# Optimization experiments

Hardware: AMD Instinct MI355X
Metric: run time of the kernel (lower is better)

Reference implementation:

```python
import jax, jax.numpy as jnp
import numpy as np

B_, L, D = 4, 2048, 1024          # batch, seq_len, d_model
E = 2 * D                         # d_inner (expand=2)
N = 8                             # d_state
K = 4                             # d_conv
R = D // 16                       # dt_rank = 64
EPS = 1e-5


def silu(x):
    return x * jax.nn.sigmoid(x)


def setup_inputs() -> dict:
    key = jax.random.key(0)
    ks = jax.random.split(key, 8)
    s = 0.02
    inp = jax.random.normal(ks[0], (B_, L, D), jnp.float32)
    in_proj_w = jax.random.normal(ks[1], (2 * E, D), jnp.float32) * s
    conv_w = jax.random.normal(ks[2], (E, 1, K), jnp.float32) * s  # depthwise, OIW
    conv_b = jnp.zeros((E,), jnp.float32)
    x_proj_w = jax.random.normal(ks[3], (R + 2 * N, E), jnp.float32) * s
    dt_proj_w = jax.random.normal(ks[4], (E, R), jnp.float32) * s
    # bias so softplus(dt) gives realistic small timesteps
    dt_proj_b = jax.random.uniform(ks[5], (E,), jnp.float32, minval=-4.0, maxval=-2.0)
    # S4D-real init: A = -[1..N] per channel
    A_log = jnp.log(jnp.broadcast_to(jnp.arange(1, N + 1, dtype=jnp.float32), (E, N)))
    D_param = jnp.ones((E,), jnp.float32)
    out_proj_w = jax.random.normal(ks[6], (D, E), jnp.float32) * s
    rms_w = jnp.ones((D,), jnp.float32)
    return dict(inp=inp, in_proj_w=in_proj_w, conv_w=conv_w, conv_b=conv_b,
                x_proj_w=x_proj_w, dt_proj_w=dt_proj_w, dt_proj_b=dt_proj_b,
                A_log=A_log, D_param=D_param, out_proj_w=out_proj_w, rms_w=rms_w)


def reference(inp, in_proj_w, conv_w, conv_b, x_proj_w, dt_proj_w, dt_proj_b,
              A_log, D_param, out_proj_w, rms_w):
    b, l, d = inp.shape
    # input projection -> x (ssm branch) and z (gate branch), each (b, l, E)
    xz = inp @ in_proj_w.T
    x, z = jnp.split(xz, 2, axis=-1)
    # depthwise causal conv1d along time
    xt = x.transpose(0, 2, 1)                                   # (b, E, l)
    xc = jax.lax.conv_general_dilated(xt, conv_w, (1,), [(K - 1, 0)],
                                      feature_group_count=E)
    x = silu((xc + conv_b[None, :, None]).transpose(0, 2, 1))   # (b, l, E)
    # data-dependent SSM params
    dbc = x @ x_proj_w.T                                        # (b, l, R+2N)
    dt, Bm, Cm = jnp.split(dbc, [R, R + N], axis=-1)
    delta = jax.nn.softplus(dt @ dt_proj_w.T + dt_proj_b)       # (b, l, E)
    A = -jnp.exp(A_log)                                         # (E, N)

    def step(h, t):
        d_t, B_t, C_t, u_t = t                                  # (b,E),(b,N),(b,N),(b,E)
        dA = jnp.exp(d_t[..., None] * A)                        # (b, E, N)
        h = h * dA + (d_t * u_t)[..., None] * B_t[:, None, :]
        y = jnp.einsum('ben,bn->be', h, C_t)
        return h, y

    xs = (delta.transpose(1, 0, 2), Bm.transpose(1, 0, 2),
          Cm.transpose(1, 0, 2), x.transpose(1, 0, 2))
    h0 = jnp.zeros((b, E, N), inp.dtype)
    _, ys = jax.lax.scan(step, h0, xs)                          # ys: (l, b, E)
    y = ys.transpose(1, 0, 2) + x * D_param                     # skip term u*D
    y = y * silu(z)                                             # gating
    out = y @ out_proj_w.T                                      # (b, l, D)
    # RMSNorm
    out = out * jax.lax.rsqrt(jnp.mean(out * out, axis=-1, keepdims=True) + EPS) * rms_w
    # dropout p=0 -> identity
    return out
```

## Files before the change

### kernel.cpp

```cpp
#include <hip/hip_runtime.h>

#define LL 2048
#define EE 2048
#define DD 1024
#define NC 32
#define CH 64

typedef short bf16x8 __attribute__((ext_vector_type(8)));
typedef float f32x4 __attribute__((ext_vector_type(4)));

__device__ inline float bf2f(unsigned short u) {
    union { unsigned u; float f; } v; v.u = ((unsigned)u) << 16; return v.f;
}
__device__ inline unsigned short f2bf(float f) {
    union { float f; unsigned u; } v; v.f = f;
    unsigned r = v.u + 0x7fff + ((v.u >> 16) & 1);
    return (unsigned short)(r >> 16);
}

__device__ inline void gload_lds16(const void* g, void* lds) {
    __builtin_amdgcn_global_load_lds(
        (const __attribute__((address_space(1))) unsigned int*)g,
        (__attribute__((address_space(3))) unsigned int*)lds, 16, 0, 0);
}

template<int MODE, int BN>
__global__ __launch_bounds__(512, 2)
void gemm8p(const unsigned short* __restrict__ A,
            const unsigned short* __restrict__ Bw,
            void* __restrict__ Cout,
            const float* __restrict__ bias,
            int M, int N, int K)
{
    constexpr int NREP = BN / 64;
    constexpr int RB   = BN / 128;
    constexpr int LH   = 2 + RB;
    constexpr int NSTRIP = BN / 4;

    extern __shared__ short lds[];
    short* Asm = lds;
    short* Bsm = lds + 2 * 2 * 256 * 32;

    const int tid = threadIdx.x;
    const int w = tid >> 6, lane = tid & 63;
    const int wm = w >> 2, wn = w & 3;

    const int gx = N / BN;
    const int nwg = gx * (M / 256);
    int lin = blockIdx.y * gx + blockIdx.x;
    int swz = ((nwg & 7) == 0) ? ((lin & 7) * (nwg >> 3) + (lin >> 3)) : lin;
    const long m0 = (long)(swz / gx) * 256;
    const long n0 = (long)(swz % gx) * BN;

    const int g = (tid & 3) ^ ((tid >> 3) & 3);
    const int arow = tid >> 2;
    const unsigned short* Ag = A + (m0 + arow) * (long)K + g * 8;
    const unsigned short* Bg = Bw + (n0 + arow) * (long)K + g * 8;
    const int ldsrow = w * 16;

    auto stageA = [&](int buf, int kh, int j, int kt) {
        gload_lds16(Ag + (long)j * 128 * K + kt * 64 + kh * 32,
                    Asm + ((buf * 2 + kh) * 256 + j * 128 + ldsrow) * 32);
    };
    auto stageB = [&](int buf, int kh, int j, int kt) {
        gload_lds16(Bg + (long)j * 128 * K + kt * 64 + kh * 32,
                    Bsm + ((buf * 2 + kh) * BN + j * 128 + ldsrow) * 32);
    };

    f32x4 acc[8][NREP] = {};

    stageA(0, 0, 0, 0); stageA(0, 0, 1, 0);
#pragma unroll
    for (int j = 0; j < RB; ++j) stageB(0, 0, j, 0);
    stageA(0, 1, 0, 0); stageA(0, 1, 1, 0);
#pragma unroll
    for (int j = 0; j < RB; ++j) stageB(0, 1, j, 0);

    const int NT = K / 64;
    const int rr = lane & 15;
    const int sl = ((lane >> 4) ^ ((rr >> 1) & 3)) * 8;

    for (int t = 0; t < NT; ++t) {
        const int cur = t & 1, nxt = cur ^ 1;
        const bool more = (t + 1 < NT);

        asm volatile("s_waitcnt vmcnt(%0)" :: "i"(LH) : "memory");
        __builtin_amdgcn_s_barrier();

        const short* Ac0 = Asm + (cur * 2 + 0) * 256 * 32;
        const short* Bc0 = Bsm + (cur * 2 + 0) * BN * 32;
        if (more) { stageA(nxt, 0, 0, t + 1); stageA(nxt, 0, 1, t + 1); }
        bf16x8 a[4], b[NREP];
#pragma unroll
        for (int m = 0; m < 4; ++m)
            a[m] = *(const bf16x8*)&Ac0[(wm * 128 + m * 16 + rr) * 32 + sl];
#pragma unroll
        for (int n = 0; n < NREP; ++n)
            b[n] = *(const bf16x8*)&Bc0[(wn * NSTRIP + n * 16 + rr) * 32 + sl];
        __builtin_amdgcn_s_setprio(1);
#pragma unroll
        for (int m = 0; m < 4; ++m)
#pragma unroll
            for (int n = 0; n < NREP; ++n)
                acc[m][n] = __builtin_amdgcn_mfma_f32_16x16x32_bf16(a[m], b[n], acc[m][n], 0, 0, 0);
        __builtin_amdgcn_s_setprio(0);
        if (more) {
#pragma unroll
            for (int j = 0; j < RB; ++j) stageB(nxt, 0, j, t + 1);
        }
#pragma unroll
        for (int m = 0; m < 4; ++m)
            a[m] = *(const bf16x8*)&Ac0[(wm * 128 + 64 + m * 16 + rr) * 32 + sl];
        __builtin_amdgcn_s_setprio(1);
#pragma unroll
        for (int m = 0; m < 4; ++m)
#pragma unroll
            for (int n = 0; n < NREP; ++n)
                acc[4 + m][n] = __builtin_amdgcn_mfma_f32_16x16x32_bf16(a[m], b[n], acc[4 + m][n], 0, 0, 0);
        __builtin_amdgcn_s_setprio(0);

        if (more) { asm volatile("s_waitcnt vmcnt(%0)" :: "i"(LH) : "memory"); }
        else      { asm volatile("s_waitcnt vmcnt(0)" ::: "memory"); }
        __builtin_amdgcn_s_barrier();

        const short* Ac1 = Asm + (cur * 2 + 1) * 256 * 32;
        const short* Bc1 = Bsm + (cur * 2 + 1) * BN * 32;
        if (more) { stageA(nxt, 1, 0, t + 1); stageA(nxt, 1, 1, t + 1); }
#pragma unroll
        for (int m = 0; m < 4; ++m)
            a[m] = *(const bf16x8*)&Ac1[(wm * 128 + m * 16 + rr) * 32 + sl];
#pragma unroll
        for (int n = 0; n < NREP; ++n)
            b[n] = *(const bf16x8*)&Bc1[(wn * NSTRIP + n * 16 + rr) * 32 + sl];
        __builtin_amdgcn_s_setprio(1);
#pragma unroll
        for (int m = 0; m < 4; ++m)
#pragma unroll
            for (int n = 0; n < NREP; ++n)
                acc[m][n] = __builtin_amdgcn_mfma_f32_16x16x32_bf16(a[m], b[n], acc[m][n], 0, 0, 0);
        __builtin_amdgcn_s_setprio(0);
        if (more) {
#pragma unroll
            for (int j = 0; j < RB; ++j) stageB(nxt, 1, j, t + 1);
        }
#pragma unroll
        for (int m = 0; m < 4; ++m)
            a[m] = *(const bf16x8*)&Ac1[(wm * 128 + 64 + m * 16 + rr) * 32 + sl];
        __builtin_amdgcn_s_setprio(1);
#pragma unroll
        for (int m = 0; m < 4; ++m)
#pragma unroll
            for (int n = 0; n < NREP; ++n)
                acc[4 + m][n] = __builtin_amdgcn_mfma_f32_16x16x32_bf16(a[m], b[n], acc[4 + m][n], 0, 0, 0);
        __builtin_amdgcn_s_setprio(0);
    }

#pragma unroll
    for (int m = 0; m < 8; ++m) {
#pragma unroll
        for (int n = 0; n < NREP; ++n) {
#pragma unroll
            for (int r = 0; r < 4; ++r) {
                long row = m0 + wm * 128 + m * 16 + (lane >> 4) * 4 + r;
                long col = n0 + wn * NSTRIP + n * 16 + (lane & 15);
                float v = acc[m][n][r];
                if (MODE == 0) {
                    ((float*)Cout)[row * N + col] = v;
                } else if (MODE == 1) {
                    ((unsigned short*)Cout)[row * N + col] = f2bf(v);
                } else {
                    v += bias[col];
                    float sp = (v > 20.f) ? v : log1pf(__expf(v));
                    ((unsigned short*)Cout)[row * N + col] = f2bf(sp);
                }
            }
        }
    }
}

template<int MODE>
__global__ __launch_bounds__(256)
void gemm_bt(const unsigned short* __restrict__ A,
             const unsigned short* __restrict__ Bw,
             void* __restrict__ Cout,
             unsigned short* __restrict__ dt_out,
             int M, int N, int K)
{
    __shared__ short As[128 * 32];
    __shared__ short Bs[128 * 32];
    const int tid = threadIdx.x;
    const int wave = tid >> 6, lane = tid & 63;
    const int wm = wave >> 1, wn = wave & 1;
    const long m0 = (long)blockIdx.y * 128;
    const long n0 = (long)blockIdx.x * 128;

    f32x4 acc[4][4] = {};

    const int srow = lane >> 2;
    const int skoff = (lane & 3) * 8;
    const int c0 = wave, c1 = wave + 4;

    for (int k0 = 0; k0 < K; k0 += 32) {
        gload_lds16(A + (m0 + c0 * 16 + srow) * (long)K + k0 + skoff, &As[c0 * 16 * 32]);
        gload_lds16(A + (m0 + c1 * 16 + srow) * (long)K + k0 + skoff, &As[c1 * 16 * 32]);
        gload_lds16(Bw + (n0 + c0 * 16 + srow) * (long)K + k0 + skoff, &Bs[c0 * 16 * 32]);
        gload_lds16(Bw + (n0 + c1 * 16 + srow) * (long)K + k0 + skoff, &Bs[c1 * 16 * 32]);
        __syncthreads();

        bf16x8 af[4], bfr[4];
#pragma unroll
        for (int m = 0; m < 4; ++m)
            af[m] = *(const bf16x8*)&As[(wm * 64 + m * 16 + (lane & 15)) * 32 + (lane >> 4) * 8];
#pragma unroll
        for (int n = 0; n < 4; ++n)
            bfr[n] = *(const bf16x8*)&Bs[(wn * 64 + n * 16 + (lane & 15)) * 32 + (lane >> 4) * 8];
#pragma unroll
        for (int m = 0; m < 4; ++m)
#pragma unroll
            for (int n = 0; n < 4; ++n)
                acc[m][n] = __builtin_amdgcn_mfma_f32_16x16x32_bf16(af[m], bfr[n], acc[m][n], 0, 0, 0);
        __syncthreads();
    }

#pragma unroll
    for (int m = 0; m < 4; ++m) {
#pragma unroll
        for (int n = 0; n < 4; ++n) {
#pragma unroll
            for (int r = 0; r < 4; ++r) {
                long row = m0 + wm * 64 + m * 16 + (lane >> 4) * 4 + r;
                long col = n0 + wn * 64 + n * 16 + (lane & 15);
                float v = acc[m][n][r];
                ((float*)Cout)[row * N + col] = v;
                if (MODE == 3) {
                    if (col < 64) dt_out[row * 64 + col] = f2bf(v);
                }
            }
        }
    }
}

__global__ void cvt_f32_bf16(const float* __restrict__ in, unsigned short* __restrict__ out, long n) {
    long i = ((long)blockIdx.x * blockDim.x + threadIdx.x) * 4;
    long stride = (long)gridDim.x * blockDim.x * 4;
    for (; i < n; i += stride) {
        float4 v = *(const float4*)(in + i);
        out[i + 0] = f2bf(v.x); out[i + 1] = f2bf(v.y);
        out[i + 2] = f2bf(v.z); out[i + 3] = f2bf(v.w);
    }
}

__global__ void cvt_pad_xproj(const float* __restrict__ in, unsigned short* __restrict__ out) {
    int i = blockIdx.x * 256 + threadIdx.x;
    int r = i >> 11, c = i & 2047;
    out[i] = (r < 80) ? f2bf(in[r * 2048 + c]) : (unsigned short)0;
}

__global__ void conv_silu_k(const unsigned short* __restrict__ xz,
                            const float* __restrict__ cw,
                            const float* __restrict__ cb,
                            unsigned short* __restrict__ xc)
{
    const int e = blockIdx.y * 256 + threadIdx.x;
    const int b = blockIdx.z;
    const int l0 = blockIdx.x * 128;
    const float w0 = cw[e * 4 + 0], w1 = cw[e * 4 + 1], w2 = cw[e * 4 + 2], w3 = cw[e * 4 + 3];
    const float bias = cb[e];
    const unsigned short* xrow = xz + (long)b * LL * 4096 + e;
    unsigned short* orow = xc + (long)b * LL * 2048 + e;
    float xm3 = (l0 >= 3) ? bf2f(xrow[(long)(l0 - 3) * 4096]) : 0.f;
    float xm2 = (l0 >= 2) ? bf2f(xrow[(long)(l0 - 2) * 4096]) : 0.f;
    float xm1 = (l0 >= 1) ? bf2f(xrow[(long)(l0 - 1) * 4096]) : 0.f;
    for (int l = l0; l < l0 + 128; ++l) {
        float x0 = bf2f(xrow[(long)l * 4096]);
        float v = bias + w0 * xm3 + w1 * xm2 + w2 * xm1 + w3 * x0;
        float s = v / (1.f + __expf(-v));
        orow[(long)l * 2048] = f2bf(s);
        xm3 = xm2; xm2 = xm1; xm1 = x0;
    }
}

__global__ __launch_bounds__(256)
void scan_local(const unsigned short* __restrict__ delta,
                const unsigned short* __restrict__ xconv,
                const float* __restrict__ dbc,
                const float* __restrict__ A_log,
                float* __restrict__ hend, float* __restrict__ Ssum)
{
    const int e = blockIdx.x * 256 + threadIdx.x;
    const int c = blockIdx.y, b = blockIdx.z;
    const int l0 = c * CH;
    float An[8];
#pragma unroll
    for (int n = 0; n < 8; ++n) An[n] = -__expf(A_log[e * 8 + n]);
    float h[8] = {};
    float S = 0.f;
    const unsigned short* drow = delta + ((long)b * LL + l0) * EE + e;
    const unsigned short* urow = xconv + ((long)b * LL + l0) * EE + e;
    const float* bc = dbc + ((long)b * LL + l0) * 128;
    for (int l = 0; l < CH; ++l) {
        float d = bf2f(drow[(long)l * EE]);
        float u = bf2f(urow[(long)l * EE]);
        float du = d * u;
        S += d;
#pragma unroll
        for (int n = 0; n < 8; ++n)
            h[n] = h[n] * __expf(d * An[n]) + du * bc[l * 128 + 64 + n];
    }
    const long o = ((long)b * NC + c) * EE + e;
#pragma unroll
    for (int n = 0; n < 8; ++n) hend[o * 8 + n] = h[n];
    Ssum[o] = S;
}

__global__ __launch_bounds__(256)
void scan_combine(const float* __restrict__ hend, const float* __restrict__ Ssum,
                  const float* __restrict__ A_log, float* __restrict__ hin)
{
    const int t = blockIdx.x * 256 + threadIdx.x;
    const int b = t >> 11, e = t & 2047;
    float An[8];
#pragma unroll
    for (int n = 0; n < 8; ++n) An[n] = -__expf(A_log[e * 8 + n]);
    float h[8] = {};
    for (int c = 0; c < NC; ++c) {
        const long o = ((long)b * NC + c) * EE + e;
#pragma unroll
        for (int n = 0; n < 8; ++n) hin[o * 8 + n] = h[n];
        float S = Ssum[o];
#pragma unroll
        for (int n = 0; n < 8; ++n)
            h[n] = h[n] * __expf(An[n] * S) + hend[o * 8 + n];
    }
}

__global__ __launch_bounds__(256)
void scan_final(const unsigned short* __restrict__ delta,
                const unsigned short* __restrict__ xconv,
                const float* __restrict__ dbc,
                const unsigned short* __restrict__ xz,
                const float* __restrict__ A_log,
                const float* __restrict__ Dparam,
                const float* __restrict__ hin,
                unsigned short* __restrict__ yg)
{
    const int e = blockIdx.x * 256 + threadIdx.x;
    const int c = blockIdx.y, b = blockIdx.z;
    const int l0 = c * CH;
    float An[8];
#pragma unroll
    for (int n = 0; n < 8; ++n) An[n] = -__expf(A_log[e * 8 + n]);
    const float Dp = Dparam[e];
    float h[8];
    const long o = ((long)b * NC + c) * EE + e;
#pragma unroll
    for (int n = 0; n < 8; ++n) h[n] = hin[o * 8 + n];
    const unsigned short* drow = delta + ((long)b * LL + l0) * EE + e;
    const unsigned short* urow = xconv + ((long)b * LL + l0) * EE + e;
    const unsigned short* zrow = xz + ((long)b * LL + l0) * 4096 + 2048 + e;
    const float* bc = dbc + ((long)b * LL + l0) * 128;
    unsigned short* yrow = yg + ((long)b * LL + l0) * EE + e;
    for (int l = 0; l < CH; ++l) {
        float d = bf2f(drow[(long)l * EE]);
        float u = bf2f(urow[(long)l * EE]);
        float du = d * u;
        float y = 0.f;
#pragma unroll
        for (int n = 0; n < 8; ++n) {
            h[n] = h[n] * __expf(d * An[n]) + du * bc[l * 128 + 64 + n];
            y += h[n] * bc[l * 128 + 72 + n];
        }
        y += u * Dp;
        float z = bf2f(zrow[(long)l * 4096]);
        float g = z / (1.f + __expf(-z));
        yrow[(long)l * EE] = f2bf(y * g);
    }
}

__global__ __launch_bounds__(256)
void rmsnorm_k(const float* __restrict__ in, const float* __restrict__ w, float* __restrict__ out) {
    const int row = blockIdx.x;
    const float4* r4 = (const float4*)(in + (long)row * 1024);
    float4 v = r4[threadIdx.x];
    float ss = v.x * v.x + v.y * v.y + v.z * v.z + v.w * v.w;
#pragma unroll
    for (int m = 32; m >= 1; m >>= 1) ss += __shfl_xor(ss, m, 64);
    __shared__ float wsum[4];
    const int wave = threadIdx.x >> 6;
    if ((threadIdx.x & 63) == 0) wsum[wave] = ss;
    __syncthreads();
    float tot = wsum[0] + wsum[1] + wsum[2] + wsum[3];
    float sc = rsqrtf(tot * (1.f / 1024.f) + 1e-5f);
    float4 wv = ((const float4*)w)[threadIdx.x];
    float4 o;
    o.x = v.x * sc * wv.x; o.y = v.y * sc * wv.y;
    o.z = v.z * sc * wv.z; o.w = v.w * sc * wv.w;
    ((float4*)(out + (long)row * 1024))[threadIdx.x] = o;
}

extern "C" void kernel_launch(void* const* d_in, const int* in_sizes, int n_in,
                              void* d_out, int out_size, void* d_ws, size_t ws_size,
                              hipStream_t stream)
{
    const float* inp   = (const float*)d_in[0];
    const float* w_in  = (const float*)d_in[1];
    const float* convw = (const float*)d_in[2];
    const float* convb = (const float*)d_in[3];
    const float* w_xp  = (const float*)d_in[4];
    const float* w_dt  = (const float*)d_in[5];
    const float* b_dt  = (const float*)d_in[6];
    const float* A_log = (const float*)d_in[7];
    const float* Dp    = (const float*)d_in[8];
    const float* w_out = (const float*)d_in[9];
    const float* rmsw  = (const float*)d_in[10];

    char* ws = (char*)d_ws;
    const size_t MB = 1024 * 1024;
    unsigned short* inp_bf   = (unsigned short*)(ws + 0);
    unsigned short* win_bf   = (unsigned short*)(ws + 16 * MB);
    unsigned short* xz_bf    = (unsigned short*)(ws + 24 * MB);
    unsigned short* xconv_bf = (unsigned short*)(ws + 88 * MB);
    unsigned short* wxp_bf   = (unsigned short*)(ws + 120 * MB);
    float*          dbc      = (float*)(ws + 121 * MB);
    unsigned short* dt_bf    = (unsigned short*)(ws + 125 * MB);
    unsigned short* wdt_bf   = (unsigned short*)(ws + 126 * MB);
    unsigned short* delta_bf = (unsigned short*)(ws + 127 * MB);
    unsigned short* yg_bf    = (unsigned short*)(ws + 191 * MB);
    unsigned short* wout_bf  = (unsigned short*)(ws + 223 * MB);
    float*          hend     = (float*)(ws + 0);
    float*          hin      = (float*)(ws + 8 * MB);
    float*          Ssum     = (float*)(ws + 16 * MB);
    float*          out_pre  = (float*)(ws + 0);

    hipFuncSetAttribute((const void*)gemm8p<1, 256>, hipFuncAttributeMaxDynamicSharedMemorySize, 131072);
    hipFuncSetAttribute((const void*)gemm8p<2, 128>, hipFuncAttributeMaxDynamicSharedMemorySize, 98304);
    hipFuncSetAttribute((const void*)gemm8p<0, 128>, hipFuncAttributeMaxDynamicSharedMemorySize, 98304);

    cvt_f32_bf16<<<2048, 256, 0, stream>>>(inp, inp_bf, (long)8192 * 1024);
    cvt_f32_bf16<<<2048, 256, 0, stream>>>(w_in, win_bf, (long)4096 * 1024);
    cvt_pad_xproj<<<1024, 256, 0, stream>>>(w_xp, wxp_bf);
    cvt_f32_bf16<<<512, 256, 0, stream>>>(w_dt, wdt_bf, (long)2048 * 64);
    cvt_f32_bf16<<<2048, 256, 0, stream>>>(w_out, wout_bf, (long)1024 * 2048);

    gemm8p<1, 256><<<dim3(16, 32), 512, 131072, stream>>>(inp_bf, win_bf, xz_bf, nullptr, 8192, 4096, 1024);
    conv_silu_k<<<dim3(16, 8, 4), 256, 0, stream>>>(xz_bf, convw, convb, xconv_bf);
    gemm_bt<3><<<dim3(1, 64), 256, 0, stream>>>(xconv_bf, wxp_bf, dbc, dt_bf, 8192, 128, 2048);
    gemm8p<2, 128><<<dim3(16, 32), 512, 98304, stream>>>(dt_bf, wdt_bf, delta_bf, b_dt, 8192, 2048, 64);
    scan_local<<<dim3(8, NC, 4), 256, 0, stream>>>(delta_bf, xconv_bf, dbc, A_log, hend, Ssum);
    scan_combine<<<32, 256, 0, stream>>>(hend, Ssum, A_log, hin);
    scan_final<<<dim3(8, NC, 4), 256, 0, stream>>>(delta_bf, xconv_bf, dbc, xz_bf, A_log, Dp, hin, yg_bf);
    gemm8p<0, 128><<<dim3(8, 32), 512, 98304, stream>>>(yg_bf, wout_bf, out_pre, nullptr, 8192, 1024, 2048);
    rmsnorm_k<<<8192, 256, 0, stream>>>(out_pre, rmsw, (float*)d_out);
}
```

Measured before the change: 379.9 us.

## Split-K x_proj GEMM, fuse conversions, vectorize conv, bf16 out_proj output

The x_proj GEMM now splits K four ways across 256 blocks instead of running on 64 blocks, uses a swizzled LDS layout, and adds a reduce kernel that also emits the bf16 dt slice. The five f32-to-bf16 conversion launches are merged into one kernel with packed stores. The conv+SiLU kernel handles two channels per thread with 32-bit loads and stores. The out_proj GEMM writes bf16 instead of f32, which halves that intermediate's traffic before RMSNorm but lowers its precision.

```diff
diff --git a/kernel.cpp b/kernel.cpp
--- a/kernel.cpp
+++ b/kernel.cpp
@@ -178,42 +178,42 @@
     }
 }
 
-template<int MODE>
 __global__ __launch_bounds__(256)
-void gemm_bt(const unsigned short* __restrict__ A,
+void gemm_xp(const unsigned short* __restrict__ A,
              const unsigned short* __restrict__ Bw,
-             void* __restrict__ Cout,
-             unsigned short* __restrict__ dt_out,
-             int M, int N, int K)
+             float* __restrict__ Cout)
 {
     __shared__ short As[128 * 32];
     __shared__ short Bs[128 * 32];
     const int tid = threadIdx.x;
     const int wave = tid >> 6, lane = tid & 63;
     const int wm = wave >> 1, wn = wave & 1;
-    const long m0 = (long)blockIdx.y * 128;
-    const long n0 = (long)blockIdx.x * 128;
+    const long m0 = (long)blockIdx.x * 128;
+    const int kz = blockIdx.y;
+    float* out = Cout + (long)kz * 8192 * 128;
 
     f32x4 acc[4][4] = {};
 
     const int srow = lane >> 2;
-    const int skoff = (lane & 3) * 8;
+    const int g = (lane & 3) ^ ((srow >> 1) & 3);
     const int c0 = wave, c1 = wave + 4;
 
-    for (int k0 = 0; k0 < K; k0 += 32) {
-        gload_lds16(A + (m0 + c0 * 16 + srow) * (long)K + k0 + skoff, &As[c0 * 16 * 32]);
-        gload_lds16(A + (m0 + c1 * 16 + srow) * (long)K + k0 + skoff, &As[c1 * 16 * 32]);
-        gload_lds16(Bw + (n0 + c0 * 16 + srow) * (long)K + k0 + skoff, &Bs[c0 * 16 * 32]);
-        gload_lds16(Bw + (n0 + c1 * 16 + srow) * (long)K + k0 + skoff, &Bs[c1 * 16 * 32]);
+    for (int k0 = kz * 512; k0 < kz * 512 + 512; k0 += 32) {
+        gload_lds16(A + (m0 + c0 * 16 + srow) * 2048L + k0 + g * 8, &As[c0 * 16 * 32]);
+        gload_lds16(A + (m0 + c1 * 16 + srow) * 2048L + k0 + g * 8, &As[c1 * 16 * 32]);
+        gload_lds16(Bw + (c0 * 16 + srow) * 2048L + k0 + g * 8, &Bs[c0 * 16 * 32]);
+        gload_lds16(Bw + (c1 * 16 + srow) * 2048L + k0 + g * 8, &Bs[c1 * 16 * 32]);
         __syncthreads();
 
+        const int rr = lane & 15;
+        const int sl = ((lane >> 4) ^ ((rr >> 1) & 3)) * 8;
         bf16x8 af[4], bfr[4];
 #pragma unroll
         for (int m = 0; m < 4; ++m)
-            af[m] = *(const bf16x8*)&As[(wm * 64 + m * 16 + (lane & 15)) * 32 + (lane >> 4) * 8];
+            af[m] = *(const bf16x8*)&As[(wm * 64 + m * 16 + rr) * 32 + sl];
 #pragma unroll
         for (int n = 0; n < 4; ++n)
-            bfr[n] = *(const bf16x8*)&Bs[(wn * 64 + n * 16 + (lane & 15)) * 32 + (lane >> 4) * 8];
+            bfr[n] = *(const bf16x8*)&Bs[(wn * 64 + n * 16 + rr) * 32 + sl];
 #pragma unroll
         for (int m = 0; m < 4; ++m)
 #pragma unroll
@@ -223,37 +223,53 @@
     }
 
 #pragma unroll
-    for (int m = 0; m < 4; ++m) {
-#pragma unroll
-        for (int n = 0; n < 4; ++n) {
+    for (int m = 0; m < 4; ++m)
+#pragma unroll
+        for (int n = 0; n < 4; ++n)
 #pragma unroll
             for (int r = 0; r < 4; ++r) {
                 long row = m0 + wm * 64 + m * 16 + (lane >> 4) * 4 + r;
-                long col = n0 + wn * 64 + n * 16 + (lane & 15);
-                float v = acc[m][n][r];
-                ((float*)Cout)[row * N + col] = v;
-                if (MODE == 3) {
-                    if (col < 64) dt_out[row * 64 + col] = f2bf(v);
-                }
+                long col = wn * 64 + n * 16 + (lane & 15);
+                out[row * 128 + col] = acc[m][n][r];
             }
-        }
-    }
-}
-
-__global__ void cvt_f32_bf16(const float* __restrict__ in, unsigned short* __restrict__ out, long n) {
-    long i = ((long)blockIdx.x * blockDim.x + threadIdx.x) * 4;
-    long stride = (long)gridDim.x * blockDim.x * 4;
-    for (; i < n; i += stride) {
-        float4 v = *(const float4*)(in + i);
-        out[i + 0] = f2bf(v.x); out[i + 1] = f2bf(v.y);
-        out[i + 2] = f2bf(v.z); out[i + 3] = f2bf(v.w);
-    }
-}
-
-__global__ void cvt_pad_xproj(const float* __restrict__ in, unsigned short* __restrict__ out) {
-    int i = blockIdx.x * 256 + threadIdx.x;
-    int r = i >> 11, c = i & 2047;
-    out[i] = (r < 80) ? f2bf(in[r * 2048 + c]) : (unsigned short)0;
+}
+
+__global__ void reduce_dbc(const float* __restrict__ part,
+                           float* __restrict__ dbc,
+                           unsigned short* __restrict__ dt)
+{
+    const long i = (long)blockIdx.x * 256 + threadIdx.x;
+    float s = part[i] + part[i + 1048576] + part[i + 2 * 1048576] + part[i + 3 * 1048576];
+    dbc[i] = s;
+    const int c = (int)(i & 127);
+    if (c < 64) dt[(i >> 7) * 64 + c] = f2bf(s);
+}
+
+__device__ inline void cvt4(const float* __restrict__ in, unsigned short* __restrict__ out, long i) {
+    float4 v = ((const float4*)in)[i];
+    unsigned lo = (unsigned)f2bf(v.x) | ((unsigned)f2bf(v.y) << 16);
+    unsigned hi = (unsigned)f2bf(v.z) | ((unsigned)f2bf(v.w) << 16);
+    ((uint2*)out)[i] = make_uint2(lo, hi);
+}
+
+__global__ void cvt_all(const float* __restrict__ inp, const float* __restrict__ w_in,
+                        const float* __restrict__ w_xp, const float* __restrict__ w_dt,
+                        const float* __restrict__ w_out,
+                        unsigned short* __restrict__ o_inp, unsigned short* __restrict__ o_win,
+                        unsigned short* __restrict__ o_wxp, unsigned short* __restrict__ o_wdt,
+                        unsigned short* __restrict__ o_wout)
+{
+    const long t = (long)blockIdx.x * 256 + threadIdx.x;
+    const long gs = (long)gridDim.x * 256;
+    for (long i = t; i < 8388608 / 4; i += gs) cvt4(inp, o_inp, i);
+    for (long i = t; i < 4194304 / 4; i += gs) cvt4(w_in, o_win, i);
+    for (long i = t; i < 2097152 / 4; i += gs) cvt4(w_out, o_wout, i);
+    for (long i = t; i < 131072 / 4; i += gs) cvt4(w_dt, o_wdt, i);
+    for (long i = t; i < 262144 / 4; i += gs) {
+        const int r = (int)(i >> 9);
+        if (r < 80) cvt4(w_xp, o_wxp, i);
+        else ((uint2*)o_wxp)[i] = make_uint2(0u, 0u);
+    }
 }
 
 __global__ void conv_silu_k(const unsigned short* __restrict__ xz,
@@ -261,22 +277,30 @@
                             const float* __restrict__ cb,
                             unsigned short* __restrict__ xc)
 {
-    const int e = blockIdx.y * 256 + threadIdx.x;
+    const int ep = blockIdx.y * 256 + threadIdx.x;
+    const int e0 = ep * 2, e1 = e0 + 1;
     const int b = blockIdx.z;
     const int l0 = blockIdx.x * 128;
-    const float w0 = cw[e * 4 + 0], w1 = cw[e * 4 + 1], w2 = cw[e * 4 + 2], w3 = cw[e * 4 + 3];
-    const float bias = cb[e];
-    const unsigned short* xrow = xz + (long)b * LL * 4096 + e;
-    unsigned short* orow = xc + (long)b * LL * 2048 + e;
-    float xm3 = (l0 >= 3) ? bf2f(xrow[(long)(l0 - 3) * 4096]) : 0.f;
-    float xm2 = (l0 >= 2) ? bf2f(xrow[(long)(l0 - 2) * 4096]) : 0.f;
-    float xm1 = (l0 >= 1) ? bf2f(xrow[(long)(l0 - 1) * 4096]) : 0.f;
+    const float wa0 = cw[e0 * 4], wa1 = cw[e0 * 4 + 1], wa2 = cw[e0 * 4 + 2], wa3 = cw[e0 * 4 + 3];
+    const float wb0 = cw[e1 * 4], wb1 = cw[e1 * 4 + 1], wb2 = cw[e1 * 4 + 2], wb3 = cw[e1 * 4 + 3];
+    const float ba = cb[e0], bb = cb[e1];
+    const unsigned* xrow = (const unsigned*)(xz + (long)b * LL * 4096) + ep;
+    unsigned* orow = (unsigned*)(xc + (long)b * LL * 2048) + ep;
+
+    float a3 = 0.f, a2 = 0.f, a1 = 0.f, b3 = 0.f, b2 = 0.f, b1 = 0.f;
+    if (l0 >= 3) { unsigned u = xrow[(long)(l0 - 3) * 2048]; a3 = bf2f(u & 0xffff); b3 = bf2f(u >> 16); }
+    if (l0 >= 2) { unsigned u = xrow[(long)(l0 - 2) * 2048]; a2 = bf2f(u & 0xffff); b2 = bf2f(u >> 16); }
+    if (l0 >= 1) { unsigned u = xrow[(long)(l0 - 1) * 2048]; a1 = bf2f(u & 0xffff); b1 = bf2f(u >> 16); }
     for (int l = l0; l < l0 + 128; ++l) {
-        float x0 = bf2f(xrow[(long)l * 4096]);
-        float v = bias + w0 * xm3 + w1 * xm2 + w2 * xm1 + w3 * x0;
-        float s = v / (1.f + __expf(-v));
-        orow[(long)l * 2048] = f2bf(s);
-        xm3 = xm2; xm2 = xm1; xm1 = x0;
+        unsigned u = xrow[(long)l * 2048];
+        float xa = bf2f(u & 0xffff), xb = bf2f(u >> 16);
+        float va = ba + wa0 * a3 + wa1 * a2 + wa2 * a1 + wa3 * xa;
+        float vb = bb + wb0 * b3 + wb1 * b2 + wb2 * b1 + wb3 * xb;
+        float sa = va / (1.f + __expf(-va));
+        float sb = vb / (1.f + __expf(-vb));
+        orow[(long)l * 1024] = (unsigned)f2bf(sa) | ((unsigned)f2bf(sb) << 16);
+        a3 = a2; a2 = a1; a1 = xa;
+        b3 = b2; b2 = b1; b1 = xb;
     }
 }
 
@@ -378,11 +402,14 @@
 }
 
 __global__ __launch_bounds__(256)
-void rmsnorm_k(const float* __restrict__ in, const float* __restrict__ w, float* __restrict__ out) {
+void rmsnorm_k(const unsigned short* __restrict__ in, const float* __restrict__ w,
+               float* __restrict__ out)
+{
     const int row = blockIdx.x;
-    const float4* r4 = (const float4*)(in + (long)row * 1024);
-    float4 v = r4[threadIdx.x];
-    float ss = v.x * v.x + v.y * v.y + v.z * v.z + v.w * v.w;
+    uint2 v2 = *(const uint2*)(in + (long)row * 1024 + threadIdx.x * 4);
+    float x0 = bf2f(v2.x & 0xffff), x1 = bf2f(v2.x >> 16);
+    float x2 = bf2f(v2.y & 0xffff), x3 = bf2f(v2.y >> 16);
+    float ss = x0 * x0 + x1 * x1 + x2 * x2 + x3 * x3;
 #pragma unroll
     for (int m = 32; m >= 1; m >>= 1) ss += __shfl_xor(ss, m, 64);
     __shared__ float wsum[4];
@@ -393,8 +420,8 @@
     float sc = rsqrtf(tot * (1.f / 1024.f) + 1e-5f);
     float4 wv = ((const float4*)w)[threadIdx.x];
     float4 o;
-    o.x = v.x * sc * wv.x; o.y = v.y * sc * wv.y;
-    o.z = v.z * sc * wv.z; o.w = v.w * sc * wv.w;
+    o.x = x0 * sc * wv.x; o.y = x1 * sc * wv.y;
+    o.z = x2 * sc * wv.z; o.w = x3 * sc * wv.w;
     ((float4*)(out + (long)row * 1024))[threadIdx.x] = o;
 }
 
@@ -427,28 +454,27 @@
     unsigned short* delta_bf = (unsigned short*)(ws + 127 * MB);
     unsigned short* yg_bf    = (unsigned short*)(ws + 191 * MB);
     unsigned short* wout_bf  = (unsigned short*)(ws + 223 * MB);
+    float*          dbc_part = (float*)(ws + 0);
     float*          hend     = (float*)(ws + 0);
     float*          hin      = (float*)(ws + 8 * MB);
     float*          Ssum     = (float*)(ws + 16 * MB);
-    float*          out_pre  = (float*)(ws + 0);
+    unsigned short* out_pre  = (unsigned short*)(ws + 0);
 
     hipFuncSetAttribute((const void*)gemm8p<1, 256>, hipFuncAttributeMaxDynamicSharedMemorySize, 131072);
     hipFuncSetAttribute((const void*)gemm8p<2, 128>, hipFuncAttributeMaxDynamicSharedMemorySize, 98304);
-    hipFuncSetAttribute((const void*)gemm8p<0, 128>, hipFuncAttributeMaxDynamicSharedMemorySize, 98304);
-
-    cvt_f32_bf16<<<2048, 256, 0, stream>>>(inp, inp_bf, (long)8192 * 1024);
-    cvt_f32_bf16<<<2048, 256, 0, stream>>>(w_in, win_bf, (long)4096 * 1024);
-    cvt_pad_xproj<<<1024, 256, 0, stream>>>(w_xp, wxp_bf);
-    cvt_f32_bf16<<<512, 256, 0, stream>>>(w_dt, wdt_bf, (long)2048 * 64);
-    cvt_f32_bf16<<<2048, 256, 0, stream>>>(w_out, wout_bf, (long)1024 * 2048);
+    hipFuncSetAttribute((const void*)gemm8p<1, 128>, hipFuncAttributeMaxDynamicSharedMemorySize, 98304);
+
+    cvt_all<<<2048, 256, 0, stream>>>(inp, w_in, w_xp, w_dt, w_out,
+                                      inp_bf, win_bf, wxp_bf, wdt_bf, wout_bf);
 
     gemm8p<1, 256><<<dim3(16, 32), 512, 131072, stream>>>(inp_bf, win_bf, xz_bf, nullptr, 8192, 4096, 1024);
-    conv_silu_k<<<dim3(16, 8, 4), 256, 0, stream>>>(xz_bf, convw, convb, xconv_bf);
-    gemm_bt<3><<<dim3(1, 64), 256, 0, stream>>>(xconv_bf, wxp_bf, dbc, dt_bf, 8192, 128, 2048);
+    conv_silu_k<<<dim3(16, 4, 4), 256, 0, stream>>>(xz_bf, convw, convb, xconv_bf);
+    gemm_xp<<<dim3(64, 4), 256, 0, stream>>>(xconv_bf, wxp_bf, dbc_part);
+    reduce_dbc<<<4096, 256, 0, stream>>>(dbc_part, dbc, dt_bf);
     gemm8p<2, 128><<<dim3(16, 32), 512, 98304, stream>>>(dt_bf, wdt_bf, delta_bf, b_dt, 8192, 2048, 64);
     scan_local<<<dim3(8, NC, 4), 256, 0, stream>>>(delta_bf, xconv_bf, dbc, A_log, hend, Ssum);
     scan_combine<<<32, 256, 0, stream>>>(hend, Ssum, A_log, hin);
     scan_final<<<dim3(8, NC, 4), 256, 0, stream>>>(delta_bf, xconv_bf, dbc, xz_bf, A_log, Dp, hin, yg_bf);
-    gemm8p<0, 128><<<dim3(8, 32), 512, 98304, stream>>>(yg_bf, wout_bf, out_pre, nullptr, 8192, 1024, 2048);
+    gemm8p<1, 128><<<dim3(8, 32), 512, 98304, stream>>>(yg_bf, wout_bf, out_pre, nullptr, 8192, 1024, 2048);
     rmsnorm_k<<<8192, 256, 0, stream>>>(out_pre, rmsw, (float*)d_out);
 }
```

Result: faster. 358.9 us (-5.5%).
